# Kernel tuning notes

Measured on AMD Instinct MI355X. Metric: run time of the kernel, lower is better.

## Reference

```python
import jax, jax.numpy as jnp
import numpy as np

N = 100000   # nodes
E = 1600000  # edges (before self loops)
B = 64       # graphs in batch
F_IN = 128
H1, C1 = 8, 8   # conv1: heads=8, per-head channels=8 -> concat out 64
H2, C2 = 1, 8   # conv2: heads=1, out=8, concat=False


def gat_conv(x, src, dst, W, att_src, att_dst, bias, H, C, concat, n_nodes):
    """PyG GATConv (shared src/dst weight, leaky_relu slope 0.2, segment softmax).
    src/dst already include self loops. x: [N, F], W: [F, H*C],
    att_src/att_dst: [1, H, C], bias: [H*C] or [C]."""
    xh = (x @ W).reshape(n_nodes, H, C)                      # [N, H, C]
    a_src = jnp.sum(xh * att_src, axis=-1)                   # [N, H]
    a_dst = jnp.sum(xh * att_dst, axis=-1)                   # [N, H]
    alpha = jax.nn.leaky_relu(a_src[src] + a_dst[dst], 0.2)  # [E', H]
    # numerically stable segment softmax over incoming edges of each dst node
    amax = jax.ops.segment_max(jax.lax.stop_gradient(alpha), dst, num_segments=n_nodes)
    ex = jnp.exp(alpha - amax[dst])
    denom = jax.ops.segment_sum(ex, dst, num_segments=n_nodes)
    alpha = ex / (denom[dst] + 1e-16)                        # [E', H]
    msg = xh[src] * alpha[..., None]                         # [E', H, C]
    out = jax.ops.segment_sum(msg, dst, num_segments=n_nodes)  # [N, H, C]
    out = out.reshape(n_nodes, H * C) if concat else out.mean(axis=1)
    return out + bias


def setup_inputs() -> dict:
    key = jax.random.key(0)
    ks = jax.random.split(key, 12)
    x = jax.random.normal(ks[0], (N, F_IN), dtype=jnp.float32)
    edge_index = jax.random.randint(ks[1], (2, E), 0, N, dtype=jnp.int32)
    batch = jnp.sort(jax.random.randint(ks[2], (N,), 0, B, dtype=jnp.int32))
    g = 0.1
    W1 = jax.random.normal(ks[3], (F_IN, H1 * C1), dtype=jnp.float32) * g
    a1_src = jax.random.normal(ks[4], (1, H1, C1), dtype=jnp.float32) * g
    a1_dst = jax.random.normal(ks[5], (1, H1, C1), dtype=jnp.float32) * g
    b1 = jnp.zeros((H1 * C1,), dtype=jnp.float32)
    W2 = jax.random.normal(ks[6], (H1 * C1, H2 * C2), dtype=jnp.float32) * g
    a2_src = jax.random.normal(ks[7], (1, H2, C2), dtype=jnp.float32) * g
    a2_dst = jax.random.normal(ks[8], (1, H2, C2), dtype=jnp.float32) * g
    b2 = jnp.zeros((C2,), dtype=jnp.float32)
    return {"x": x, "edge_index": edge_index, "batch": batch,
            "W1": W1, "a1_src": a1_src, "a1_dst": a1_dst, "b1": b1,
            "W2": W2, "a2_src": a2_src, "a2_dst": a2_dst, "b2": b2}


def reference(x, edge_index, batch, W1, a1_src, a1_dst, b1, W2, a2_src, a2_dst, b2):
    # add self loops (PyG GATConv default)
    loop = jnp.arange(N, dtype=edge_index.dtype)
    src = jnp.concatenate([edge_index[0], loop])
    dst = jnp.concatenate([edge_index[1], loop])
    # eval mode: dropouts are identity
    h = gat_conv(x, src, dst, W1, a1_src, a1_dst, b1, H1, C1, True, N)
    h = jax.nn.elu(h)
    h = gat_conv(h, src, dst, W2, a2_src, a2_dst, b2, H2, C2, False, N)
    # global mean pool over graphs
    sums = jax.ops.segment_sum(h, batch, num_segments=B)          # [B, C2]
    cnt = jax.ops.segment_sum(jnp.ones((N,), h.dtype), batch, num_segments=B)
    return sums / jnp.maximum(cnt, 1.0)[:, None]
```

## Files before the change

### kernel.cpp

```cpp
#include <hip/hip_runtime.h>
#include <hip/hip_bf16.h>

#define BIN_SHIFT 8
#define BIN_NODES 256
#define BIN_CAP   8192
#define EPT       16

typedef float v2f __attribute__((ext_vector_type(2)));

__device__ __forceinline__ float leaky02(float a) { return fmaxf(a, 0.2f * a); }
__device__ __forceinline__ unsigned short f2bf(float f) {
    __hip_bfloat16 h = __float2bfloat16(f);
    return *(unsigned short*)&h;
}
__device__ __forceinline__ float bflo(unsigned u) { return __uint_as_float(u << 16); }
__device__ __forceinline__ float bfhi(unsigned u) { return __uint_as_float(u & 0xffff0000u); }
__device__ __forceinline__ v2f bf2(unsigned u) {
    v2f r; r.x = __uint_as_float(u << 16); r.y = __uint_as_float(u & 0xffff0000u); return r;
}

__global__ __launch_bounds__(512) void k1_kernel(const float* __restrict__ x,
                                                 const float* __restrict__ W,
                                                 const float* __restrict__ a1d,
                                                 const int* __restrict__ ei,
                                                 __hip_bfloat16* __restrict__ xh,
                                                 float* __restrict__ adst,
                                                 int* __restrict__ cur,
                                                 unsigned* __restrict__ binned,
                                                 int N, int E, int Etot, int NB, int NBB) {
    __shared__ float ws[128 * 64];
    __shared__ float xs[64][66];
    __shared__ int bcnt[512];
    int tid = threadIdx.x;
    if (blockIdx.x < NBB) {
        bcnt[tid] = 0;
        __syncthreads();
        long long base = (long long)blockIdx.x * 512 * EPT;
#pragma unroll 4
        for (int i = 0; i < EPT; ++i) {
            long long e = base + i * 512 + tid;
            if (e < Etot) {
                int dst = (e < E) ? ei[E + e] : (int)(e - E);
                atomicAdd(&bcnt[dst >> BIN_SHIFT], 1);
            }
        }
        __syncthreads();
        for (int b = tid; b < NB; b += 512) {
            int c = bcnt[b];
            bcnt[b] = c ? atomicAdd(&cur[b], c) : 0;
        }
        __syncthreads();
#pragma unroll 4
        for (int i = 0; i < EPT; ++i) {
            long long e = base + i * 512 + tid;
            if (e < Etot) {
                int src, dst;
                if (e < E) { src = ei[e]; dst = ei[E + e]; }
                else       { src = dst = (int)(e - E); }
                int bin = dst >> BIN_SHIFT;
                int p = atomicAdd(&bcnt[bin], 1);
                if (p < BIN_CAP)
                    binned[(size_t)bin * BIN_CAP + p] = ((unsigned)(dst & (BIN_NODES - 1)) << 24) | (unsigned)src;
            }
        }
        return;
    }
    int gb = blockIdx.x - NBB;
    for (int i = tid; i < 2048; i += 512) ((float4*)ws)[i] = ((const float4*)W)[i];
    int row0 = gb * 64;
    int tc = tid & 15, tr = tid >> 4;
    float acc[2][4] = {};
#pragma unroll
    for (int half = 0; half < 2; ++half) {
        __syncthreads();
        for (int i = tid; i < 1024; i += 512) {
            int r = i >> 4, c4 = i & 15;
            int row = row0 + r;
            float4 v = make_float4(0.f, 0.f, 0.f, 0.f);
            if (row < N) v = ((const float4*)x)[(size_t)row * 32 + half * 16 + c4];
            float* p = &xs[r][c4 * 4];
            p[0] = v.x; p[1] = v.y; p[2] = v.z; p[3] = v.w;
        }
        __syncthreads();
#pragma unroll 4
        for (int k = 0; k < 64; ++k) {
            float a0 = xs[tr * 2][k];
            float a1 = xs[tr * 2 + 1][k];
            float4 b = *(const float4*)&ws[(half * 64 + k) * 64 + tc * 4];
            acc[0][0] += a0 * b.x; acc[0][1] += a0 * b.y; acc[0][2] += a0 * b.z; acc[0][3] += a0 * b.w;
            acc[1][0] += a1 * b.x; acc[1][1] += a1 * b.y; acc[1][2] += a1 * b.z; acc[1][3] += a1 * b.w;
        }
    }
    float4 dv = ((const float4*)a1d)[tc];
    int head = tc >> 1;
#pragma unroll
    for (int r = 0; r < 2; ++r) {
        int row = row0 + tr * 2 + r;
        if (row < N) {
            uint2 o;
            o.x = (unsigned)f2bf(acc[r][0]) | ((unsigned)f2bf(acc[r][1]) << 16);
            o.y = (unsigned)f2bf(acc[r][2]) | ((unsigned)f2bf(acc[r][3]) << 16);
            *(uint2*)(xh + (size_t)row * 64 + tc * 4) = o;
        }
        float dp = acc[r][0] * dv.x + acc[r][1] * dv.y + acc[r][2] * dv.z + acc[r][3] * dv.w;
        dp += __shfl_xor(dp, 1);
        if (!(tc & 1) && row < N) adst[row * 8 + head] = dp;
    }
}

__global__ __launch_bounds__(256) void binC_kernel(const int* __restrict__ cur,
                                                   const unsigned* __restrict__ binned,
                                                   int* __restrict__ rowptr,
                                                   int* __restrict__ esrc,
                                                   int N, int Etot, int NB) {
    int bin = blockIdx.x;
    int tid = threadIdx.x;
    __shared__ int psum[256];
    __shared__ int sc[256];
    __shared__ int ndc[256];
    int s = 0;
    for (int i = tid; i < bin; i += 256) s += cur[i];
    psum[tid] = s;
    __syncthreads();
    for (int off = 128; off > 0; off >>= 1) {
        if (tid < off) psum[tid] += psum[tid + off];
        __syncthreads();
    }
    int bbase = psum[0];
    int cnt = cur[bin];
    ndc[tid] = 0;
    __syncthreads();
    const unsigned* bp = binned + (size_t)bin * BIN_CAP;
    for (int i = tid; i < cnt; i += 256)
        atomicAdd(&ndc[bp[i] >> 24], 1);
    __syncthreads();
    int v = ndc[tid];
    sc[tid] = v;
    __syncthreads();
    for (int off = 1; off < 256; off <<= 1) {
        int t = (tid >= off) ? sc[tid - off] : 0;
        __syncthreads();
        sc[tid] += t;
        __syncthreads();
    }
    int excl = sc[tid] - v;
    int node = bin * BIN_NODES + tid;
    if (node < N) rowptr[node] = bbase + excl;
    if (bin == NB - 1 && tid == 0) rowptr[N] = Etot;
    ndc[tid] = excl;
    __syncthreads();
    for (int i = tid; i < cnt; i += 256) {
        unsigned w = bp[i];
        int p = atomicAdd(&ndc[w >> 24], 1);
        esrc[bbase + p] = (int)(w & 0xFFFFFFu);
    }
}

__global__ __launch_bounds__(256) void agg1_kernel(const int* __restrict__ rowptr,
                                                   const int* __restrict__ esrc,
                                                   const float* __restrict__ a1s,
                                                   const float* __restrict__ adst,
                                                   const __hip_bfloat16* __restrict__ xh,
                                                   const float* __restrict__ b1,
                                                   __hip_bfloat16* __restrict__ h1, int N) {
    int node = blockIdx.x * 4 + (threadIdx.x >> 6);
    if (node >= N) return;
    int lane = threadIdx.x & 63;
    unsigned slot = (unsigned)(lane >> 3), h = (unsigned)(lane & 7);
    float adh = adst[(unsigned)node * 8u + h];
    const float* wsh = a1s + h * 8u;
    v2f w01 = {wsh[0], wsh[1]}, w23 = {wsh[2], wsh[3]};
    v2f w45 = {wsh[4], wsh[5]}, w67 = {wsh[6], wsh[7]};
    unsigned start = (unsigned)rowptr[node];
    int len = rowptr[node + 1] - (int)start;
    const uint4* xh4 = (const uint4*)xh;
    float d = 0.f;
    v2f acc0 = {0.f, 0.f}, acc1 = {0.f, 0.f}, acc2 = {0.f, 0.f}, acc3 = {0.f, 0.f};
    for (int kb = 0; kb < len; kb += 32) {
        int k0 = kb + (int)slot;
        bool ok0 = k0 < len, ok1 = k0 + 8 < len, ok2 = k0 + 16 < len, ok3 = k0 + 24 < len;
        unsigned s0 = ok0 ? (unsigned)esrc[start + k0] : 0u;
        unsigned s1 = ok1 ? (unsigned)esrc[start + k0 + 8] : 0u;
        unsigned s2 = ok2 ? (unsigned)esrc[start + k0 + 16] : 0u;
        unsigned s3 = ok3 ? (unsigned)esrc[start + k0 + 24] : 0u;
        uint4 u0 = xh4[s0 * 8u + h];
        uint4 u1 = xh4[s1 * 8u + h];
        uint4 u2 = xh4[s2 * 8u + h];
        uint4 u3 = xh4[s3 * 8u + h];
        v2f v00 = bf2(u0.x), v01 = bf2(u0.y), v02 = bf2(u0.z), v03 = bf2(u0.w);
        v2f v10 = bf2(u1.x), v11 = bf2(u1.y), v12 = bf2(u1.z), v13 = bf2(u1.w);
        v2f v20 = bf2(u2.x), v21 = bf2(u2.y), v22 = bf2(u2.z), v23 = bf2(u2.w);
        v2f v30 = bf2(u3.x), v31 = bf2(u3.y), v32 = bf2(u3.z), v33 = bf2(u3.w);
        v2f av0 = v00 * w01 + v01 * w23 + v02 * w45 + v03 * w67;
        v2f av1 = v10 * w01 + v11 * w23 + v12 * w45 + v13 * w67;
        v2f av2 = v20 * w01 + v21 * w23 + v22 * w45 + v23 * w67;
        v2f av3 = v30 * w01 + v31 * w23 + v32 * w45 + v33 * w67;
        float p0 = ok0 ? __expf(leaky02(av0.x + av0.y + adh)) : 0.f;
        float p1 = ok1 ? __expf(leaky02(av1.x + av1.y + adh)) : 0.f;
        float p2 = ok2 ? __expf(leaky02(av2.x + av2.y + adh)) : 0.f;
        float p3 = ok3 ? __expf(leaky02(av3.x + av3.y + adh)) : 0.f;
        d += (p0 + p1) + (p2 + p3);
        acc0 += v00 * p0; acc1 += v01 * p0; acc2 += v02 * p0; acc3 += v03 * p0;
        acc0 += v10 * p1; acc1 += v11 * p1; acc2 += v12 * p1; acc3 += v13 * p1;
        acc0 += v20 * p2; acc1 += v21 * p2; acc2 += v22 * p2; acc3 += v23 * p2;
        acc0 += v30 * p3; acc1 += v31 * p3; acc2 += v32 * p3; acc3 += v33 * p3;
    }
#pragma unroll
    for (int off = 8; off < 64; off <<= 1) {
        d += __shfl_xor(d, off);
        acc0.x += __shfl_xor(acc0.x, off); acc0.y += __shfl_xor(acc0.y, off);
        acc1.x += __shfl_xor(acc1.x, off); acc1.y += __shfl_xor(acc1.y, off);
        acc2.x += __shfl_xor(acc2.x, off); acc2.y += __shfl_xor(acc2.y, off);
        acc3.x += __shfl_xor(acc3.x, off); acc3.y += __shfl_xor(acc3.y, off);
    }
    float vals[8] = {acc0.x, acc0.y, acc1.x, acc1.y, acc2.x, acc2.y, acc3.x, acc3.y};
    float hv = vals[0];
#pragma unroll
    for (int c = 1; c < 8; ++c) hv = ((int)slot == c) ? vals[c] : hv;
    int f = (int)(h * 8u + slot);
    hv = hv / (d + 1e-16f) + b1[f];
    hv = hv > 0.f ? hv : __expf(hv) - 1.0f;
    float hvp = __shfl(hv, ((lane & 7) << 3) | (lane >> 3));
    h1[(unsigned)node * 64u + (unsigned)lane] = __float2bfloat16(hvp);
}

__global__ __launch_bounds__(256) void gemm2h_kernel(const __hip_bfloat16* __restrict__ h1,
                                                     const float* __restrict__ W2,
                                                     const float* __restrict__ a2d,
                                                     __hip_bfloat16* __restrict__ xh2,
                                                     float* __restrict__ adst2, int N) {
    __shared__ float w2s[512];
    __shared__ float aa[8];
    int tid = threadIdx.x;
    for (int i = tid; i < 512; i += 256) w2s[i] = W2[i];
    if (tid < 8) aa[tid] = a2d[tid];
    __syncthreads();
    unsigned n = blockIdx.x * 256u + (unsigned)tid;
    if (n >= (unsigned)N) return;
    const uint4* hp = (const uint4*)h1 + n * 8u;
    float q[8] = {};
#pragma unroll
    for (int j = 0; j < 8; ++j) {
        uint4 u = hp[j];
        float hv[8] = {bflo(u.x), bfhi(u.x), bflo(u.y), bfhi(u.y),
                       bflo(u.z), bfhi(u.z), bflo(u.w), bfhi(u.w)};
#pragma unroll
        for (int e = 0; e < 8; ++e) {
            int f = j * 8 + e;
            float4 wa = *(const float4*)&w2s[f * 8];
            float4 wb = *(const float4*)&w2s[f * 8 + 4];
            q[0] += hv[e] * wa.x; q[1] += hv[e] * wa.y;
            q[2] += hv[e] * wa.z; q[3] += hv[e] * wa.w;
            q[4] += hv[e] * wb.x; q[5] += hv[e] * wb.y;
            q[6] += hv[e] * wb.z; q[7] += hv[e] * wb.w;
        }
    }
    uint4 o;
    o.x = (unsigned)f2bf(q[0]) | ((unsigned)f2bf(q[1]) << 16);
    o.y = (unsigned)f2bf(q[2]) | ((unsigned)f2bf(q[3]) << 16);
    o.z = (unsigned)f2bf(q[4]) | ((unsigned)f2bf(q[5]) << 16);
    o.w = (unsigned)f2bf(q[6]) | ((unsigned)f2bf(q[7]) << 16);
    *((uint4*)xh2 + n) = o;
    float d2 = 0.f;
#pragma unroll
    for (int c = 0; c < 8; ++c) d2 += q[c] * aa[c];
    adst2[n] = d2;
}

__global__ __launch_bounds__(256) void agg2_pool_kernel(const int* __restrict__ rowptr,
                                                        const int* __restrict__ esrc,
                                                        const float* __restrict__ a2s,
                                                        const float* __restrict__ adst2,
                                                        const __hip_bfloat16* __restrict__ xh2,
                                                        const float* __restrict__ b2,
                                                        const int* __restrict__ batch,
                                                        float* __restrict__ pool,
                                                        float* __restrict__ cnt, int N, int B) {
    __shared__ float ps[64 * 8];
    __shared__ float cs[64];
    int tid = threadIdx.x;
    for (int i = tid; i < 512; i += 256) ps[i] = 0.f;
    if (tid < 64) cs[tid] = 0.f;
    __syncthreads();
    int node = blockIdx.x * 32 + (tid >> 3);
    int slot = tid & 7;
    if (node < N) {
        float adh = adst2[node];
        v2f w01 = {a2s[0], a2s[1]}, w23 = {a2s[2], a2s[3]};
        v2f w45 = {a2s[4], a2s[5]}, w67 = {a2s[6], a2s[7]};
        unsigned start = (unsigned)rowptr[node];
        int len = rowptr[node + 1] - (int)start;
        const uint4* x4 = (const uint4*)xh2;
        float d = 0.f;
        v2f acc0 = {0.f, 0.f}, acc1 = {0.f, 0.f}, acc2 = {0.f, 0.f}, acc3 = {0.f, 0.f};
        for (int kb = 0; kb < len; kb += 32) {
            int k0 = kb + slot;
            bool ok0 = k0 < len, ok1 = k0 + 8 < len, ok2 = k0 + 16 < len, ok3 = k0 + 24 < len;
            unsigned s0 = ok0 ? (unsigned)esrc[start + k0] : 0u;
            unsigned s1 = ok1 ? (unsigned)esrc[start + k0 + 8] : 0u;
            unsigned s2 = ok2 ? (unsigned)esrc[start + k0 + 16] : 0u;
            unsigned s3 = ok3 ? (unsigned)esrc[start + k0 + 24] : 0u;
            uint4 u0 = x4[s0];
            uint4 u1 = x4[s1];
            uint4 u2 = x4[s2];
            uint4 u3 = x4[s3];
            v2f v00 = bf2(u0.x), v01 = bf2(u0.y), v02 = bf2(u0.z), v03 = bf2(u0.w);
            v2f v10 = bf2(u1.x), v11 = bf2(u1.y), v12 = bf2(u1.z), v13 = bf2(u1.w);
            v2f v20 = bf2(u2.x), v21 = bf2(u2.y), v22 = bf2(u2.z), v23 = bf2(u2.w);
            v2f v30 = bf2(u3.x), v31 = bf2(u3.y), v32 = bf2(u3.z), v33 = bf2(u3.w);
            v2f av0 = v00 * w01 + v01 * w23 + v02 * w45 + v03 * w67;
            v2f av1 = v10 * w01 + v11 * w23 + v12 * w45 + v13 * w67;
            v2f av2 = v20 * w01 + v21 * w23 + v22 * w45 + v23 * w67;
            v2f av3 = v30 * w01 + v31 * w23 + v32 * w45 + v33 * w67;
            float p0 = ok0 ? __expf(leaky02(av0.x + av0.y + adh)) : 0.f;
            float p1 = ok1 ? __expf(leaky02(av1.x + av1.y + adh)) : 0.f;
            float p2 = ok2 ? __expf(leaky02(av2.x + av2.y + adh)) : 0.f;
            float p3 = ok3 ? __expf(leaky02(av3.x + av3.y + adh)) : 0.f;
            d += (p0 + p1) + (p2 + p3);
            acc0 += v00 * p0; acc1 += v01 * p0; acc2 += v02 * p0; acc3 += v03 * p0;
            acc0 += v10 * p1; acc1 += v11 * p1; acc2 += v12 * p1; acc3 += v13 * p1;
            acc0 += v20 * p2; acc1 += v21 * p2; acc2 += v22 * p2; acc3 += v23 * p2;
            acc0 += v30 * p3; acc1 += v31 * p3; acc2 += v32 * p3; acc3 += v33 * p3;
        }
#pragma unroll
        for (int off = 1; off < 8; off <<= 1) {
            d += __shfl_xor(d, off);
            acc0.x += __shfl_xor(acc0.x, off); acc0.y += __shfl_xor(acc0.y, off);
            acc1.x += __shfl_xor(acc1.x, off); acc1.y += __shfl_xor(acc1.y, off);
            acc2.x += __shfl_xor(acc2.x, off); acc2.y += __shfl_xor(acc2.y, off);
            acc3.x += __shfl_xor(acc3.x, off); acc3.y += __shfl_xor(acc3.y, off);
        }
        float vals[8] = {acc0.x, acc0.y, acc1.x, acc1.y, acc2.x, acc2.y, acc3.x, acc3.y};
        float v = vals[0];
#pragma unroll
        for (int c = 1; c < 8; ++c) v = (slot == c) ? vals[c] : v;
        v = v / (d + 1e-16f) + b2[slot];
        int b = batch[node];
        atomicAdd(&ps[b * 8 + slot], v);
        if (slot == 0) atomicAdd(&cs[b], 1.0f);
    }
    __syncthreads();
    for (int i = tid; i < 512; i += 256)
        if (ps[i] != 0.f) atomicAdd(&pool[i], ps[i]);
    if (tid < 64 && cs[tid] != 0.f) atomicAdd(&cnt[tid], cs[tid]);
}

__global__ __launch_bounds__(256) void final_kernel(const float* __restrict__ pool,
                                                    const float* __restrict__ cnt,
                                                    float* __restrict__ out, int B) {
    int idx = blockIdx.x * 256 + threadIdx.x;
    if (idx >= B * 8) return;
    out[idx] = pool[idx] / fmaxf(cnt[idx >> 3], 1.0f);
}

extern "C" void kernel_launch(void* const* d_in, const int* in_sizes, int n_in,
                              void* d_out, int out_size, void* d_ws, size_t ws_size,
                              hipStream_t stream) {
    const float* x   = (const float*)d_in[0];
    const int*   ei  = (const int*)d_in[1];
    const int*   bat = (const int*)d_in[2];
    const float* W1  = (const float*)d_in[3];
    const float* a1s = (const float*)d_in[4];
    const float* a1d = (const float*)d_in[5];
    const float* b1  = (const float*)d_in[6];
    const float* W2  = (const float*)d_in[7];
    const float* a2s = (const float*)d_in[8];
    const float* a2d = (const float*)d_in[9];
    const float* b2  = (const float*)d_in[10];
    float* out = (float*)d_out;

    const int N = in_sizes[0] / 128;
    const int E = in_sizes[1] / 2;
    const int B = out_size / 8;
    const int Etot = E + N;
    const int NB = (N + BIN_NODES - 1) / BIN_NODES;
    const int NBB = (Etot + 512 * EPT - 1) / (512 * EPT);
    const int NG = (N + 63) / 64;

    float* wsp = (float*)d_ws;
    __hip_bfloat16* xh1 = (__hip_bfloat16*)wsp;
    float* adst1  = wsp + (size_t)N * 32;
    __hip_bfloat16* h1 = (__hip_bfloat16*)(adst1 + (size_t)N * 8);
    __hip_bfloat16* xh2 = (__hip_bfloat16*)(adst1 + (size_t)N * 40);
    float* adst2  = adst1 + (size_t)N * 44;
    int*   rowptr = (int*)(adst2 + (size_t)N);
    int*   esrc   = rowptr + (size_t)N + 8;
    unsigned* binned = (unsigned*)(esrc + (size_t)Etot);
    int*   cur    = (int*)(binned + (size_t)NB * BIN_CAP);
    float* pool   = (float*)(cur + NB);
    float* cnt    = pool + (size_t)B * 8;
    size_t zbytes = ((size_t)NB + 9 * (size_t)B) * 4;
    hipMemsetAsync(cur, 0, zbytes, stream);

    k1_kernel<<<dim3(NBB + NG), dim3(512), 0, stream>>>(x, W1, a1d, ei,
                                                        xh1, adst1,
                                                        cur, binned, N, E, Etot, NB, NBB);
    binC_kernel<<<dim3(NB), dim3(256), 0, stream>>>(cur, binned, rowptr, esrc, N, Etot, NB);
    agg1_kernel<<<dim3((N + 3) / 4), dim3(256), 0, stream>>>(rowptr, esrc, a1s, adst1, xh1, b1, h1, N);
    gemm2h_kernel<<<dim3((N + 255) / 256), dim3(256), 0, stream>>>(h1, W2, a2d, xh2, adst2, N);
    agg2_pool_kernel<<<dim3((N + 31) / 32), dim3(256), 0, stream>>>(rowptr, esrc, a2s, adst2,
                                                                    xh2, b2, bat, pool, cnt, N, B);
    final_kernel<<<dim3((B * 8 + 255) / 256), dim3(256), 0, stream>>>(pool, cnt, out, B);
}
```

Baseline: 147.2 us.

## Cache dst in LDS, vectorize GEMM LDS reads, fuse final divide into pool kernel

The binning blocks now keep dst indices in the otherwise idle weight LDS buffer, so the second pass skips a global reload of edge destinations. The layer-1 GEMM stages x rows with float4 stores and reads them as float4 over a padded row stride, which cuts LDS instruction count. The final mean division moves into the last block of agg2_pool through a completion counter and threadfence, removing one kernel launch. In exchange it adds a global atomic and fences at the end of every pool block.

```diff
diff --git a/kernel.cpp b/kernel.cpp
--- a/kernel.cpp
+++ b/kernel.cpp
@@ -29,10 +29,11 @@
                                                  unsigned* __restrict__ binned,
                                                  int N, int E, int Etot, int NB, int NBB) {
     __shared__ float ws[128 * 64];
-    __shared__ float xs[64][66];
+    __shared__ float xs[64][68];
     __shared__ int bcnt[512];
     int tid = threadIdx.x;
     if (blockIdx.x < NBB) {
+        int* dstbuf = (int*)ws;
         bcnt[tid] = 0;
         __syncthreads();
         long long base = (long long)blockIdx.x * 512 * EPT;
@@ -41,6 +42,7 @@
             long long e = base + i * 512 + tid;
             if (e < Etot) {
                 int dst = (e < E) ? ei[E + e] : (int)(e - E);
+                dstbuf[i * 512 + tid] = dst;
                 atomicAdd(&bcnt[dst >> BIN_SHIFT], 1);
             }
         }
@@ -54,9 +56,8 @@
         for (int i = 0; i < EPT; ++i) {
             long long e = base + i * 512 + tid;
             if (e < Etot) {
-                int src, dst;
-                if (e < E) { src = ei[e]; dst = ei[E + e]; }
-                else       { src = dst = (int)(e - E); }
+                int dst = dstbuf[i * 512 + tid];
+                int src = (e < E) ? ei[e] : dst;
                 int bin = dst >> BIN_SHIFT;
                 int p = atomicAdd(&bcnt[bin], 1);
                 if (p < BIN_CAP)
@@ -78,17 +79,23 @@
             int row = row0 + r;
             float4 v = make_float4(0.f, 0.f, 0.f, 0.f);
             if (row < N) v = ((const float4*)x)[(size_t)row * 32 + half * 16 + c4];
-            float* p = &xs[r][c4 * 4];
-            p[0] = v.x; p[1] = v.y; p[2] = v.z; p[3] = v.w;
-        }
-        __syncthreads();
-#pragma unroll 4
-        for (int k = 0; k < 64; ++k) {
-            float a0 = xs[tr * 2][k];
-            float a1 = xs[tr * 2 + 1][k];
-            float4 b = *(const float4*)&ws[(half * 64 + k) * 64 + tc * 4];
-            acc[0][0] += a0 * b.x; acc[0][1] += a0 * b.y; acc[0][2] += a0 * b.z; acc[0][3] += a0 * b.w;
-            acc[1][0] += a1 * b.x; acc[1][1] += a1 * b.y; acc[1][2] += a1 * b.z; acc[1][3] += a1 * b.w;
+            *(float4*)&xs[r][c4 * 4] = v;
+        }
+        __syncthreads();
+#pragma unroll 2
+        for (int kt = 0; kt < 16; ++kt) {
+            float4 a0 = *(const float4*)&xs[tr * 2][kt * 4];
+            float4 a1 = *(const float4*)&xs[tr * 2 + 1][kt * 4];
+            float a0j[4] = {a0.x, a0.y, a0.z, a0.w};
+            float a1j[4] = {a1.x, a1.y, a1.z, a1.w};
+#pragma unroll
+            for (int j = 0; j < 4; ++j) {
+                float4 b = *(const float4*)&ws[(half * 64 + kt * 4 + j) * 64 + tc * 4];
+                acc[0][0] += a0j[j] * b.x; acc[0][1] += a0j[j] * b.y;
+                acc[0][2] += a0j[j] * b.z; acc[0][3] += a0j[j] * b.w;
+                acc[1][0] += a1j[j] * b.x; acc[1][1] += a1j[j] * b.y;
+                acc[1][2] += a1j[j] * b.z; acc[1][3] += a1j[j] * b.w;
+            }
         }
     }
     float4 dv = ((const float4*)a1d)[tc];
@@ -275,9 +282,12 @@
                                                         const float* __restrict__ b2,
                                                         const int* __restrict__ batch,
                                                         float* __restrict__ pool,
-                                                        float* __restrict__ cnt, int N, int B) {
+                                                        float* __restrict__ cnt,
+                                                        int* __restrict__ done,
+                                                        float* __restrict__ out, int N, int B) {
     __shared__ float ps[64 * 8];
     __shared__ float cs[64];
+    __shared__ int amlast;
     int tid = threadIdx.x;
     for (int i = tid; i < 512; i += 256) ps[i] = 0.f;
     if (tid < 64) cs[tid] = 0.f;
@@ -343,14 +353,15 @@
     for (int i = tid; i < 512; i += 256)
         if (ps[i] != 0.f) atomicAdd(&pool[i], ps[i]);
     if (tid < 64 && cs[tid] != 0.f) atomicAdd(&cnt[tid], cs[tid]);
-}
-
-__global__ __launch_bounds__(256) void final_kernel(const float* __restrict__ pool,
-                                                    const float* __restrict__ cnt,
-                                                    float* __restrict__ out, int B) {
-    int idx = blockIdx.x * 256 + threadIdx.x;
-    if (idx >= B * 8) return;
-    out[idx] = pool[idx] / fmaxf(cnt[idx >> 3], 1.0f);
+    __threadfence();
+    __syncthreads();
+    if (tid == 0) amlast = (atomicAdd(done, 1) == (int)gridDim.x - 1);
+    __syncthreads();
+    if (amlast) {
+        __threadfence();
+        for (int i = tid; i < B * 8; i += 256)
+            out[i] = pool[i] / fmaxf(cnt[i >> 3], 1.0f);
+    }
 }
 
 extern "C" void kernel_launch(void* const* d_in, const int* in_sizes, int n_in,
@@ -389,7 +400,8 @@
     int*   cur    = (int*)(binned + (size_t)NB * BIN_CAP);
     float* pool   = (float*)(cur + NB);
     float* cnt    = pool + (size_t)B * 8;
-    size_t zbytes = ((size_t)NB + 9 * (size_t)B) * 4;
+    int*   done   = (int*)(cnt + B);
+    size_t zbytes = ((size_t)NB + 9 * (size_t)B + 1) * 4;
     hipMemsetAsync(cur, 0, zbytes, stream);
 
     k1_kernel<<<dim3(NBB + NG), dim3(512), 0, stream>>>(x, W1, a1d, ei,
@@ -399,6 +411,6 @@
     agg1_kernel<<<dim3((N + 3) / 4), dim3(256), 0, stream>>>(rowptr, esrc, a1s, adst1, xh1, b1, h1, N);
     gemm2h_kernel<<<dim3((N + 255) / 256), dim3(256), 0, stream>>>(h1, W2, a2d, xh2, adst2, N);
     agg2_pool_kernel<<<dim3((N + 31) / 32), dim3(256), 0, stream>>>(rowptr, esrc, a2s, adst2,
-                                                                    xh2, b2, bat, pool, cnt, N, B);
-    final_kernel<<<dim3((B * 8 + 255) / 256), dim3(256), 0, stream>>>(pool, cnt, out, B);
-}
+                                                                    xh2, b2, bat, pool, cnt,
+                                                                    done, out, N, B);
+}
```

Measured after the change: 329.7 us. 2.24x slower.
